# Performance work log

Measured on AMD Instinct MI355X. Metric: run time of the kernel, lower is better.

## Reference

```python
import jax, jax.numpy as jnp
import numpy as np

D_MODEL = 1024
NUM_SLOTS = 4096
MIN_K = 8
MAX_K = 32


def setup_inputs() -> dict:
    key = jax.random.key(0)
    k1, k2, k3 = jax.random.split(key, 3)
    x = jax.random.normal(k1, (4, 1024, D_MODEL), dtype=jnp.float32)
    param_pool = 0.02 * jax.random.normal(k2, (NUM_SLOTS, D_MODEL), dtype=jnp.float32)
    w_router = 0.02 * jax.random.normal(k3, (D_MODEL, NUM_SLOTS), dtype=jnp.float32)
    return {"x": x, "param_pool": param_pool, "w_router": w_router}


def _route(x, w_router):
    # Router: linear projection to slot logits, softmax, dynamic top-k in [MIN_K, MAX_K].
    logits = jnp.einsum('bsd,dn->bsn', x, w_router)           # [B,S,N]
    probs = jax.nn.softmax(logits, axis=-1)
    top_probs, indices = jax.lax.top_k(probs, MAX_K)          # [B,S,K]
    # dynamic k: always keep first MIN_K slots; keep up to MAX_K while prob > uniform
    pos = jnp.arange(MAX_K)
    keep = (pos < MIN_K) | (top_probs > (1.0 / NUM_SLOTS))    # [B,S,K] bool
    keep_f = keep.astype(top_probs.dtype)
    masked = top_probs * keep_f
    weights = masked / (jnp.sum(masked, axis=-1, keepdims=True) + 1e-9)
    # load-balancing aux loss: N * sum(mean_prob_per_slot * frac_tokens_routed_per_slot)
    mean_probs = jnp.mean(probs, axis=(0, 1))                 # [N]
    counts = jnp.zeros((NUM_SLOTS,), dtype=jnp.float32).at[indices.reshape(-1)].add(keep_f.reshape(-1))
    frac = counts / (jnp.sum(keep_f) + 1e-9)
    aux_loss = NUM_SLOTS * jnp.sum(mean_probs * frac)
    return indices, weights, keep, aux_loss


def reference(x, param_pool, w_router):
    indices, weights, keep, aux_loss = _route(x, w_router)
    selected_params = param_pool[indices]                      # [B,S,K,D] gather
    proj = jnp.einsum('bsd,bskd->bsk', x, selected_params)     # per-token dot scores
    weighted_proj = proj * weights
    output = jnp.einsum('bsk,bskd->bsd', weighted_proj, selected_params)
    flat_indices = indices.reshape(-1)
    flat_keep = keep.reshape(-1)
    touched = jnp.zeros((NUM_SLOTS,), dtype=jnp.bool_).at[flat_indices].max(flat_keep)
    active_count = jnp.sum(touched)
    return (output, aux_loss, active_count)
```

## Files before the change

### kernel.cpp

```cpp
#include <hip/hip_runtime.h>
#include <math.h>
#include <stdint.h>

#define D_MODEL   1024
#define NUM_SLOTS 4096
#define N_TOKENS  4096
#define MIN_K     8
#define MAX_K     32
#define KP        1024
#define NSTEP     32

typedef _Float16 f16x8 __attribute__((ext_vector_type(8)));
typedef _Float16 f16x4 __attribute__((ext_vector_type(4)));
typedef float    f32x4 __attribute__((ext_vector_type(4)));

__device__ __forceinline__ void gload16(const void* g, void* l) {
    __builtin_amdgcn_global_load_lds((const __attribute__((address_space(1))) void*)g,
                                     (__attribute__((address_space(3))) void*)l,
                                     16, 0, 0);
}

__device__ __forceinline__ uint32_t bf16rn(float f) {
    uint32_t u = __float_as_uint(f);
    return (u + 0x7FFFu + ((u >> 16) & 1u)) >> 16;
}

__device__ __forceinline__ uint32_t ford(float f) {
    uint32_t b = __float_as_uint(f);
    return b ^ (uint32_t)(((int32_t)b >> 31) | 0x80000000);
}

__global__ __launch_bounds__(256) void pack_all(const float* __restrict__ x,
                                                const float* __restrict__ w,
                                                const float* __restrict__ pool,
                                                _Float16* __restrict__ A,
                                                _Float16* __restrict__ BT,
                                                uint32_t* __restrict__ poolbf,
                                                float* __restrict__ clr,
                                                int* __restrict__ failcnt) {
    __shared__ float tile[64][65];
    const int bid = blockIdx.x;
    const int tid = threadIdx.x;

    if (bid < 4096) {
        if (bid < 32) clr[bid * 256 + tid] = 0.f;
        if (bid == 32 && tid == 0) *failcnt = 0;
        const int i = bid * 256 + tid;
        const float4 v = reinterpret_cast<const float4*>(x)[i];
        const int t = i >> 8;
        const int d = (i & 255) << 2;
        f16x4 hi;
        hi[0] = (_Float16)v.x; hi[1] = (_Float16)v.y;
        hi[2] = (_Float16)v.z; hi[3] = (_Float16)v.w;
        *(f16x4*)(A + (size_t)t * KP + d) = hi;
    } else if (bid < 5120) {
        const int b2 = bid - 4096;
        const int n0 = (b2 & 63) * 64;
        const int k0 = (b2 >> 6) * 64;
        {
            const int c  = tid & 63;
            const int r0 = tid >> 6;
#pragma unroll
            for (int i = 0; i < 16; ++i) {
                const int r = r0 * 16 + i;
                tile[r][c] = w[(size_t)(k0 + r) * NUM_SLOTS + n0 + c];
            }
        }
        __syncthreads();
        const int nl  = tid >> 2;
        const int kl0 = (tid & 3) * 16;
        _Float16* rowp = BT + (size_t)(n0 + nl) * KP + k0;
#pragma unroll
        for (int j4 = 0; j4 < 16; j4 += 4) {
            f16x4 hi;
#pragma unroll
            for (int u = 0; u < 4; ++u)
                hi[u] = (_Float16)tile[kl0 + j4 + u][nl];
            *(f16x4*)(rowp + kl0 + j4) = hi;
        }
    } else {
        const size_t i = (size_t)(bid - 5120) * 256 + tid;
        const float4* s4 = reinterpret_cast<const float4*>(pool);
        const float4 a = s4[2 * i];
        const float4 b = s4[2 * i + 1];
        uint4 u;
        u.x = bf16rn(a.x) | (bf16rn(a.y) << 16);
        u.y = bf16rn(a.z) | (bf16rn(a.w) << 16);
        u.z = bf16rn(b.x) | (bf16rn(b.y) << 16);
        u.w = bf16rn(b.z) | (bf16rn(b.w) << 16);
        reinterpret_cast<uint4*>(poolbf)[i] = u;
    }
}

#define STAGE_A(NXT, S2) \
    gload16(gA0 + (size_t)(S2) * 32, (void*)(AsF + (NXT) * 8192 + tid * 8)); \
    gload16(gA1 + (size_t)(S2) * 32, (void*)(AsF + (NXT) * 8192 + 4096 + tid * 8));
#define STAGE_B(NXT, S2) \
    gload16(gB0 + (size_t)(S2) * 32, (void*)(BsF + (NXT) * 8192 + tid * 8)); \
    gload16(gB1 + (size_t)(S2) * 32, (void*)(BsF + (NXT) * 8192 + 4096 + tid * 8));

#define MM(AF, M) \
    acc[M][0] = __builtin_amdgcn_mfma_f32_16x16x32_f16(AF, bf0, acc[M][0], 0, 0, 0); \
    acc[M][1] = __builtin_amdgcn_mfma_f32_16x16x32_f16(AF, bf1, acc[M][1], 0, 0, 0); \
    acc[M][2] = __builtin_amdgcn_mfma_f32_16x16x32_f16(AF, bf2, acc[M][2], 0, 0, 0); \
    acc[M][3] = __builtin_amdgcn_mfma_f32_16x16x32_f16(AF, bf3, acc[M][3], 0, 0, 0);

#define GSTEP(S, CUR, NXT) do { \
    const _Float16* a_ = AsF + (CUR) * 8192; \
    const _Float16* b_ = BsF + (CUR) * 8192; \
    f16x8 bf0 = *(const f16x8*)(b_ + offB0); \
    f16x8 bf1 = *(const f16x8*)(b_ + offB1); \
    f16x8 bf2 = *(const f16x8*)(b_ + offB2); \
    f16x8 bf3 = *(const f16x8*)(b_ + offB3); \
    f16x8 a0 = *(const f16x8*)(a_ + offA0); \
    f16x8 a1 = *(const f16x8*)(a_ + offA1); \
    f16x8 a2 = *(const f16x8*)(a_ + offA2); \
    f16x8 a3 = *(const f16x8*)(a_ + offA3); \
    if ((S) + 2 < NSTEP) { STAGE_A(NXT, (S) + 2) } \
    asm volatile("" ::: "memory"); \
    __builtin_amdgcn_s_barrier(); \
    __builtin_amdgcn_s_setprio(1); \
    MM(a0, 0) MM(a1, 1) MM(a2, 2) MM(a3, 3) \
    __builtin_amdgcn_s_setprio(0); \
    asm volatile("" ::: "memory"); \
    __builtin_amdgcn_s_barrier(); \
    a0 = *(const f16x8*)(a_ + offA4); \
    a1 = *(const f16x8*)(a_ + offA5); \
    a2 = *(const f16x8*)(a_ + offA6); \
    a3 = *(const f16x8*)(a_ + offA7); \
    if ((S) + 2 < NSTEP) { STAGE_B(NXT, (S) + 2) } \
    asm volatile("" ::: "memory"); \
    __builtin_amdgcn_s_barrier(); \
    __builtin_amdgcn_s_setprio(1); \
    MM(a0, 4) MM(a1, 5) MM(a2, 6) MM(a3, 7) \
    __builtin_amdgcn_s_setprio(0); \
    if ((S) < NSTEP - 2) { asm volatile("s_waitcnt vmcnt(4)" ::: "memory"); } \
    else                 { asm volatile("s_waitcnt vmcnt(0)" ::: "memory"); } \
    __builtin_amdgcn_s_barrier(); \
} while (0)

__global__ __launch_bounds__(512, 2) void gemm256(const _Float16* __restrict__ A,
                                                  const _Float16* __restrict__ BT,
                                                  float* __restrict__ C,
                                                  int nbm) {
    __shared__ _Float16 AsF[4 * 8192];
    __shared__ _Float16 BsF[4 * 8192];
    const int tid  = threadIdx.x;
    const int lane = tid & 63;
    const int wv   = tid >> 6;
    const int wm   = wv >> 2;
    const int wn   = wv & 3;

    int brow, bcol;
    {
        const int bid = blockIdx.x;
        if (nbm == 16) {
            const int xcd = bid & 7;
            const int l   = bid >> 3;
            brow = (xcd & 3) * 4 + (l & 3);
            bcol = (xcd >> 2) * 8 + (l >> 2);
        } else {
            brow = bid >> 4;
            bcol = bid & 15;
        }
    }
    const size_t bm = (size_t)brow * 256;
    const size_t bn = (size_t)bcol * 256;

    const int rowA = tid >> 2;
    const int slot = tid & 3;
    const int sswz = slot ^ ((rowA >> 1) & 3);
    const _Float16* gA0 = A  + (bm + rowA) * (size_t)KP + sswz * 8;
    const _Float16* gA1 = A  + (bm + rowA + 128) * (size_t)KP + sswz * 8;
    const _Float16* gB0 = BT + (bn + rowA) * (size_t)KP + sswz * 8;
    const _Float16* gB1 = BT + (bn + rowA + 128) * (size_t)KP + sswz * 8;

    int offA0, offA1, offA2, offA3, offA4, offA5, offA6, offA7;
    int offB0, offB1, offB2, offB3;
    {
        const int r15 = lane & 15, ls = lane >> 4;
#define AOFF(M) (((wm) * 128 + (M) * 16 + r15) * 32 + \
                 ((ls ^ ((((wm) * 128 + (M) * 16 + r15) >> 1) & 3)) * 8))
#define BOFF(N) (((wn) * 64 + (N) * 16 + r15) * 32 + \
                 ((ls ^ ((((wn) * 64 + (N) * 16 + r15) >> 1) & 3)) * 8))
        offA0 = AOFF(0); offA1 = AOFF(1); offA2 = AOFF(2); offA3 = AOFF(3);
        offA4 = AOFF(4); offA5 = AOFF(5); offA6 = AOFF(6); offA7 = AOFF(7);
        offB0 = BOFF(0); offB1 = BOFF(1); offB2 = BOFF(2); offB3 = BOFF(3);
#undef AOFF
#undef BOFF
    }

    f32x4 acc[8][4] = {};

    STAGE_A(0, 0) STAGE_B(0, 0)
    STAGE_A(1, 1) STAGE_B(1, 1)
    asm volatile("s_waitcnt vmcnt(4)" ::: "memory");
    __builtin_amdgcn_s_barrier();

    for (int s4 = 0; s4 < NSTEP; s4 += 4) {
        GSTEP(s4 + 0, 0, 2);
        GSTEP(s4 + 1, 1, 3);
        GSTEP(s4 + 2, 2, 0);
        GSTEP(s4 + 3, 3, 1);
    }

    const size_t crow = bm + wm * 128 + ((lane >> 4) << 2);
    const size_t ccol = bn + wn * 64 + (lane & 15);
#pragma unroll
    for (int m = 0; m < 8; ++m)
#pragma unroll
        for (int r = 0; r < 4; ++r) {
            float* cp = C + (crow + m * 16 + r) * (size_t)NUM_SLOTS + ccol;
#pragma unroll
            for (int n = 0; n < 4; ++n) cp[n * 16] = acc[m][n][r];
        }
}

#define RECOMP(G, A, B, Cc, D) do { \
    uint32_t t0 = (msk & (1u << (A)))  ? k##A  : 0u; \
    uint32_t t1 = (msk & (1u << (B)))  ? k##B  : 0u; \
    uint32_t t2 = (msk & (1u << (Cc))) ? k##Cc : 0u; \
    uint32_t t3 = (msk & (1u << (D)))  ? k##D  : 0u; \
    t0 = t0 > t1 ? t0 : t1; t2 = t2 > t3 ? t2 : t3; \
    gm##G = t0 > t2 ? t0 : t2; } while (0)

#define XROUND(IT) do { \
    uint32_t best = gm0; \
    if (gm1 > best) best = gm1; \
    if (gm2 > best) best = gm2; \
    if (gm3 > best) best = gm3; \
    uint32_t wb = best; \
    _Pragma("unroll") \
    for (int o = 32; o; o >>= 1) { \
        const uint32_t p = __shfl_xor(wb, o); \
        if (p > wb) wb = p; \
    } \
    if (lane == (IT)) kept = wb; \
    if (best == wb) { \
        const int idx = 4095 - (int)(wb & 0xFFFu); \
        const int rem = idx - kb; \
        const int jj = rem >> 8; \
        msk &= ~(1u << (4 * jj + (rem & 3))); \
        switch (jj) { \
            case 0:  RECOMP(0, 0, 1, 2, 3); break; \
            case 1:  RECOMP(1, 4, 5, 6, 7); break; \
            case 2:  RECOMP(2, 8, 9, 10, 11); break; \
            default: RECOMP(3, 12, 13, 14, 15); break; \
        } \
    } \
} while (0)

#define MAKEKEYS(E0, E1, E2, E3) \
    k0  = (ford((E0).x) & 0xFFFFF000u) | (uint32_t)(4095 - (kb + 0)); \
    k1  = (ford((E0).y) & 0xFFFFF000u) | (uint32_t)(4095 - (kb + 1)); \
    k2  = (ford((E0).z) & 0xFFFFF000u) | (uint32_t)(4095 - (kb + 2)); \
    k3  = (ford((E0).w) & 0xFFFFF000u) | (uint32_t)(4095 - (kb + 3)); \
    k4  = (ford((E1).x) & 0xFFFFF000u) | (uint32_t)(4095 - (kb + 256)); \
    k5  = (ford((E1).y) & 0xFFFFF000u) | (uint32_t)(4095 - (kb + 257)); \
    k6  = (ford((E1).z) & 0xFFFFF000u) | (uint32_t)(4095 - (kb + 258)); \
    k7  = (ford((E1).w) & 0xFFFFF000u) | (uint32_t)(4095 - (kb + 259)); \
    k8  = (ford((E2).x) & 0xFFFFF000u) | (uint32_t)(4095 - (kb + 512)); \
    k9  = (ford((E2).y) & 0xFFFFF000u) | (uint32_t)(4095 - (kb + 513)); \
    k10 = (ford((E2).z) & 0xFFFFF000u) | (uint32_t)(4095 - (kb + 514)); \
    k11 = (ford((E2).w) & 0xFFFFF000u) | (uint32_t)(4095 - (kb + 515)); \
    k12 = (ford((E3).x) & 0xFFFFF000u) | (uint32_t)(4095 - (kb + 768)); \
    k13 = (ford((E3).y) & 0xFFFFF000u) | (uint32_t)(4095 - (kb + 769)); \
    k14 = (ford((E3).z) & 0xFFFFF000u) | (uint32_t)(4095 - (kb + 770)); \
    k15 = (ford((E3).w) & 0xFFFFF000u) | (uint32_t)(4095 - (kb + 771));

#define UNPK8(q, a0,a1,a2,a3,a4,a5,a6,a7) \
    a0 = __uint_as_float((q).x << 16); a1 = __uint_as_float((q).x & 0xFFFF0000u); \
    a2 = __uint_as_float((q).y << 16); a3 = __uint_as_float((q).y & 0xFFFF0000u); \
    a4 = __uint_as_float((q).z << 16); a5 = __uint_as_float((q).z & 0xFFFF0000u); \
    a6 = __uint_as_float((q).w << 16); a7 = __uint_as_float((q).w & 0xFFFF0000u);

#define PROJ_AND_OUT(TOK) do { \
    const float4* x4 = reinterpret_cast<const float4*>(x + (size_t)(TOK) * D_MODEL); \
    const float4 xa0 = x4[2 * lane]; \
    const float4 xb0 = x4[2 * lane + 1]; \
    const float4 xa1 = x4[2 * lane + 128]; \
    const float4 xb1 = x4[2 * lane + 129]; \
    float4 oa0 = {0,0,0,0}, ob0 = {0,0,0,0}, oa1 = {0,0,0,0}, ob1 = {0,0,0,0}; \
    _Pragma("unroll") \
    for (int ii = 0; ii < 8; ++ii) { \
        const int   i     = w * 8 + ii; \
        const int   slotg = __shfl(slotv, i); \
        const float wgt   = __shfl(wgtl, i); \
        if (wgt != 0.f) { \
            const uint4* pr = reinterpret_cast<const uint4*>(poolbf + (size_t)slotg * (D_MODEL / 2)); \
            const uint4 q0 = pr[lane]; \
            const uint4 q1 = pr[lane + 64]; \
            float pA0,pA1,pA2,pA3,pA4,pA5,pA6,pA7; \
            float pB0,pB1,pB2,pB3,pB4,pB5,pB6,pB7; \
            UNPK8(q0, pA0,pA1,pA2,pA3,pA4,pA5,pA6,pA7) \
            UNPK8(q1, pB0,pB1,pB2,pB3,pB4,pB5,pB6,pB7) \
            float d; \
            d = xa0.x * pA0; \
            d = fmaf(xa0.y, pA1, d); d = fmaf(xa0.z, pA2, d); d = fmaf(xa0.w, pA3, d); \
            d = fmaf(xb0.x, pA4, d); d = fmaf(xb0.y, pA5, d); d = fmaf(xb0.z, pA6, d); d = fmaf(xb0.w, pA7, d); \
            d = fmaf(xa1.x, pB0, d); d = fmaf(xa1.y, pB1, d); d = fmaf(xa1.z, pB2, d); d = fmaf(xa1.w, pB3, d); \
            d = fmaf(xb1.x, pB4, d); d = fmaf(xb1.y, pB5, d); d = fmaf(xb1.z, pB6, d); d = fmaf(xb1.w, pB7, d); \
            _Pragma("unroll") \
            for (int o = 32; o; o >>= 1) d += __shfl_xor(d, o); \
            const float wp = d * wgt; \
            oa0.x = fmaf(wp, pA0, oa0.x); oa0.y = fmaf(wp, pA1, oa0.y); \
            oa0.z = fmaf(wp, pA2, oa0.z); oa0.w = fmaf(wp, pA3, oa0.w); \
            ob0.x = fmaf(wp, pA4, ob0.x); ob0.y = fmaf(wp, pA5, ob0.y); \
            ob0.z = fmaf(wp, pA6, ob0.z); ob0.w = fmaf(wp, pA7, ob0.w); \
            oa1.x = fmaf(wp, pB0, oa1.x); oa1.y = fmaf(wp, pB1, oa1.y); \
            oa1.z = fmaf(wp, pB2, oa1.z); oa1.w = fmaf(wp, pB3, oa1.w); \
            ob1.x = fmaf(wp, pB4, ob1.x); ob1.y = fmaf(wp, pB5, ob1.y); \
            ob1.z = fmaf(wp, pB6, ob1.z); ob1.w = fmaf(wp, pB7, ob1.w); \
        } \
    } \
    { \
        float4* op = reinterpret_cast<float4*>(s_union + w * 1024); \
        op[2 * lane]       = oa0; \
        op[2 * lane + 1]   = ob0; \
        op[2 * lane + 128] = oa1; \
        op[2 * lane + 129] = ob1; \
    } \
    __syncthreads(); \
    float4 r = {0, 0, 0, 0}; \
    _Pragma("unroll") \
    for (int ww = 0; ww < 4; ++ww) { \
        const float4 vv = reinterpret_cast<const float4*>(s_union + ww * 1024)[tid]; \
        r.x += vv.x; r.y += vv.y; r.z += vv.z; r.w += vv.w; \
    } \
    reinterpret_cast<float4*>(out + (size_t)(TOK) * D_MODEL)[tid] = r; \
} while (0)

__global__ __launch_bounds__(256) void router_kernel(
    const float* __restrict__ logits,
    const float* __restrict__ x,
    const uint32_t* __restrict__ poolbf,
    float* __restrict__ out,
    float2* __restrict__ minv,
    float* __restrict__ counts,
    int* __restrict__ failcnt,
    int* __restrict__ faillist) {
    __shared__ float    s_union[NUM_SLOTS];
    __shared__ uint32_t s_cand[68];
    __shared__ float    s_redv[4];

    const int tid  = threadIdx.x;
    const int w    = tid >> 6;
    const int lane = tid & 63;
    const int wseg = w << 10;
    const int t    = blockIdx.x;

    const float4* lrow4 =
        reinterpret_cast<const float4*>(logits + (size_t)t * NUM_SLOTS + wseg);

    float4 lv0, lv1, lv2, lv3;
    lv0 = lrow4[lane];
    lv1 = lrow4[lane + 64];
    lv2 = lrow4[lane + 128];
    lv3 = lrow4[lane + 192];
    reinterpret_cast<float4*>(s_union + wseg)[lane]       = lv0;
    reinterpret_cast<float4*>(s_union + wseg)[lane + 64]  = lv1;
    reinterpret_cast<float4*>(s_union + wseg)[lane + 128] = lv2;
    reinterpret_cast<float4*>(s_union + wseg)[lane + 192] = lv3;
    float lmax = fmaxf(fmaxf(fmaxf(lv0.x, lv0.y), fmaxf(lv0.z, lv0.w)),
                       fmaxf(fmaxf(lv1.x, lv1.y), fmaxf(lv1.z, lv1.w)));
    lmax = fmaxf(lmax, fmaxf(fmaxf(lv2.x, lv2.y), fmaxf(lv2.z, lv2.w)));
    lmax = fmaxf(lmax, fmaxf(fmaxf(lv3.x, lv3.y), fmaxf(lv3.z, lv3.w)));
#pragma unroll
    for (int o = 32; o; o >>= 1) lmax = fmaxf(lmax, __shfl_xor(lmax, o));
    if (lane == 0) s_redv[w] = lmax;
    __syncthreads();
    const float m = fmaxf(fmaxf(s_redv[0], s_redv[1]), fmaxf(s_redv[2], s_redv[3]));
    __syncthreads();

    float lsum;
    {
        float4 ev0, ev1, ev2, ev3;
        ev0.x = __expf(lv0.x - m); ev0.y = __expf(lv0.y - m);
        ev0.z = __expf(lv0.z - m); ev0.w = __expf(lv0.w - m);
        ev1.x = __expf(lv1.x - m); ev1.y = __expf(lv1.y - m);
        ev1.z = __expf(lv1.z - m); ev1.w = __expf(lv1.w - m);
        ev2.x = __expf(lv2.x - m); ev2.y = __expf(lv2.y - m);
        ev2.z = __expf(lv2.z - m); ev2.w = __expf(lv2.w - m);
        ev3.x = __expf(lv3.x - m); ev3.y = __expf(lv3.y - m);
        ev3.z = __expf(lv3.z - m); ev3.w = __expf(lv3.w - m);
        lsum = (ev0.x + ev0.y + ev0.z + ev0.w) + (ev1.x + ev1.y + ev1.z + ev1.w) +
               (ev2.x + ev2.y + ev2.z + ev2.w) + (ev3.x + ev3.y + ev3.z + ev3.w);
    }
#pragma unroll
    for (int o = 32; o; o >>= 1) lsum += __shfl_xor(lsum, o);
    if (lane == 0) s_redv[w] = lsum;
    __syncthreads();
    const float inv = 1.0f / (s_redv[0] + s_redv[1] + s_redv[2] + s_redv[3]);
    if (tid == 0) minv[t] = make_float2(m, inv);

    const int kb = wseg + 4 * lane;
    uint32_t k0, k1, k2, k3, k4, k5, k6, k7;
    uint32_t k8, k9, k10, k11, k12, k13, k14, k15;
    MAKEKEYS(lv0, lv1, lv2, lv3)

    uint32_t msk = 0xFFFFu;
    uint32_t gm0, gm1, gm2, gm3;
    RECOMP(0, 0, 1, 2, 3); RECOMP(1, 4, 5, 6, 7);
    RECOMP(2, 8, 9, 10, 11); RECOMP(3, 12, 13, 14, 15);

    uint32_t kept = 0;
    for (int it = 0; it < 16; ++it) { XROUND(it); }

    {
        uint32_t best = gm0;
        if (gm1 > best) best = gm1;
        if (gm2 > best) best = gm2;
        if (gm3 > best) best = gm3;
#pragma unroll
        for (int o = 32; o; o >>= 1) {
            const uint32_t p = __shfl_xor(best, o);
            if (p > best) best = p;
        }
        if (lane == 0) s_cand[64 + w] = best;
    }
    if (lane < 16) s_cand[w * 16 + lane] = kept;
    __syncthreads();

    uint32_t v0 = s_cand[lane];
#pragma unroll
    for (int k = 2; k <= 64; k <<= 1) {
#pragma unroll
        for (int j = k >> 1; j > 0; j >>= 1) {
            const bool jl = (lane & j) == 0;
            const uint32_t p = __shfl_xor(v0, j);
            const bool km = ((lane & k) == 0) == jl;
            v0 = ((p > v0) == km) ? p : v0;
        }
    }

    const uint32_t th = __shfl(v0, 31);
    uint32_t mw = s_cand[64];
    {
        const uint32_t m1 = s_cand[65], m2 = s_cand[66], m3 = s_cand[67];
        if (m1 > mw) mw = m1;
        if (m2 > mw) mw = m2;
        if (m3 > mw) mw = m3;
    }
    if (th < mw) {
        if (tid == 0) {
            const int fi = atomicAdd(failcnt, 1);
            faillist[fi] = t;
        }
        return;
    }

    const int slotv = 4095 - (int)(v0 & 0xFFFu);
    float pv = 0.f;
    if (lane < 32) pv = __expf(s_union[slotv] - m) * inv;
    const bool kp = (lane < MIN_K) || (pv > (1.0f / 4096.0f));
    float wsum = kp ? pv : 0.f;
#pragma unroll
    for (int o = 32; o; o >>= 1) wsum += __shfl_xor(wsum, o);
    const float wgtl = kp ? pv / (wsum + 1e-9f) : 0.f;
    if (w == 0 && lane < 32 && kp) atomicAdd(&counts[slotv], 1.0f);
    __syncthreads();

    PROJ_AND_OUT(t);
}

__global__ __launch_bounds__(256) void router_fixup(
    const float* __restrict__ logits,
    const float* __restrict__ x,
    const uint32_t* __restrict__ poolbf,
    float* __restrict__ out,
    const float2* __restrict__ minv,
    float* __restrict__ counts,
    const int* __restrict__ failcnt,
    const int* __restrict__ faillist) {
    __shared__ float    s_union[NUM_SLOTS];
    __shared__ uint32_t s_cand[128];

    const int tid  = threadIdx.x;
    const int w    = tid >> 6;
    const int lane = tid & 63;
    const int wseg = w << 10;
    const int n    = failcnt[0];

    for (int fi = blockIdx.x; fi < n; fi += gridDim.x) {
        const int t = faillist[fi];
        const float4* lrow4 =
            reinterpret_cast<const float4*>(logits + (size_t)t * NUM_SLOTS + wseg);
        const float4 lv0 = lrow4[lane];
        const float4 lv1 = lrow4[lane + 64];
        const float4 lv2 = lrow4[lane + 128];
        const float4 lv3 = lrow4[lane + 192];
        reinterpret_cast<float4*>(s_union + wseg)[lane]       = lv0;
        reinterpret_cast<float4*>(s_union + wseg)[lane + 64]  = lv1;
        reinterpret_cast<float4*>(s_union + wseg)[lane + 128] = lv2;
        reinterpret_cast<float4*>(s_union + wseg)[lane + 192] = lv3;
        const float2 mv = minv[t];
        const float m = mv.x, inv = mv.y;

        const int kb = wseg + 4 * lane;
        uint32_t k0, k1, k2, k3, k4, k5, k6, k7;
        uint32_t k8, k9, k10, k11, k12, k13, k14, k15;
        MAKEKEYS(lv0, lv1, lv2, lv3)

        uint32_t msk = 0xFFFFu;
        uint32_t gm0, gm1, gm2, gm3;
        RECOMP(0, 0, 1, 2, 3); RECOMP(1, 4, 5, 6, 7);
        RECOMP(2, 8, 9, 10, 11); RECOMP(3, 12, 13, 14, 15);

        uint32_t kept = 0;
        for (int it = 0; it < 32; ++it) { XROUND(it); }
        if (lane < 32) s_cand[w * 32 + lane] = kept;
        __syncthreads();

        uint32_t v0 = s_cand[lane];
        uint32_t v1 = s_cand[64 + lane];
#pragma unroll
        for (int k = 2; k <= 128; k <<= 1) {
#pragma unroll
            for (int j = k >> 1; j > 0; j >>= 1) {
                if (j == 64) {
                    const uint32_t a = v0 > v1 ? v0 : v1;
                    const uint32_t b = v0 > v1 ? v1 : v0;
                    v0 = a; v1 = b;
                } else {
                    const bool jl = (lane & j) == 0;
                    {
                        const uint32_t p = __shfl_xor(v0, j);
                        const bool km = ((lane & k) == 0) == jl;
                        v0 = ((p > v0) == km) ? p : v0;
                    }
                    {
                        const uint32_t p = __shfl_xor(v1, j);
                        const bool km = (((lane + 64) & k) == 0) == jl;
                        v1 = ((p > v1) == km) ? p : v1;
                    }
                }
            }
        }

        const int slotv = 4095 - (int)(v0 & 0xFFFu);
        float pv = 0.f;
        if (lane < 32) pv = __expf(s_union[slotv] - m) * inv;
        const bool kp = (lane < MIN_K) || (pv > (1.0f / 4096.0f));
        float wsum = kp ? pv : 0.f;
#pragma unroll
        for (int o = 32; o; o >>= 1) wsum += __shfl_xor(wsum, o);
        const float wgtl = kp ? pv / (wsum + 1e-9f) : 0.f;
        if (w == 0 && lane < 32 && kp) atomicAdd(&counts[slotv], 1.0f);
        __syncthreads();

        PROJ_AND_OUT(t);
        __syncthreads();
    }
}

__global__ __launch_bounds__(256) void colsum_lg(const float* __restrict__ logits,
                                                 const float2* __restrict__ minv,
                                                 float* __restrict__ colsum) {
    const int tid = threadIdx.x;
    const int s0  = blockIdx.x * 1024;
    const int t0  = blockIdx.y * 64;
    float a0 = 0.f, a1 = 0.f, a2 = 0.f, a3 = 0.f;
    for (int t = 0; t < 64; ++t) {
        const float2 mv = minv[t0 + t];
        const float4 v = reinterpret_cast<const float4*>(
            logits + (size_t)(t0 + t) * NUM_SLOTS + s0)[tid];
        a0 = fmaf(__expf(v.x - mv.x), mv.y, a0);
        a1 = fmaf(__expf(v.y - mv.x), mv.y, a1);
        a2 = fmaf(__expf(v.z - mv.x), mv.y, a2);
        a3 = fmaf(__expf(v.w - mv.x), mv.y, a3);
    }
    const int c = s0 + 4 * tid;
    atomicAdd(&colsum[c + 0], a0);
    atomicAdd(&colsum[c + 1], a1);
    atomicAdd(&colsum[c + 2], a2);
    atomicAdd(&colsum[c + 3], a3);
}

__global__ __launch_bounds__(256) void finalize_kernel(
    const float* __restrict__ counts,
    const float* __restrict__ colsum,
    float* __restrict__ out2) {
    __shared__ float s_tot[4], s_act[4], s_dot[4];
    const int tid = threadIdx.x;
    float tot = 0.f, act = 0.f, dot = 0.f;
#pragma unroll
    for (int j = 0; j < 16; ++j) {
        const int i = j * 256 + tid;
        const float c = counts[i];
        tot += c;
        act += (c > 0.f) ? 1.f : 0.f;
        dot += colsum[i] * c;
    }
#pragma unroll
    for (int o = 32; o; o >>= 1) {
        tot += __shfl_xor(tot, o);
        act += __shfl_xor(act, o);
        dot += __shfl_xor(dot, o);
    }
    if ((tid & 63) == 0) {
        s_tot[tid >> 6] = tot; s_act[tid >> 6] = act; s_dot[tid >> 6] = dot;
    }
    __syncthreads();
    if (tid == 0) {
        const float T  = s_tot[0] + s_tot[1] + s_tot[2] + s_tot[3];
        const float A  = s_act[0] + s_act[1] + s_act[2] + s_act[3];
        const float Dt = s_dot[0] + s_dot[1] + s_dot[2] + s_dot[3];
        out2[0] = Dt / (T + 1e-9f);
        out2[1] = A;
    }
}

extern "C" void kernel_launch(void* const* d_in, const int* in_sizes, int n_in,
                              void* d_out, int out_size, void* d_ws, size_t ws_size,
                              hipStream_t stream) {
    const float* x    = (const float*)d_in[0];
    const float* pool = (const float*)d_in[1];
    const float* w    = (const float*)d_in[2];
    float* out = (float*)d_out;

    const size_t MB = 1024 * 1024;
    char* ws = (char*)d_ws;
    float*     colsum   = (float*)ws;
    float*     counts   = (float*)(ws + 16 * 1024);
    float2*    minv     = (float2*)(ws + 32 * 1024);
    int*       failcnt  = (int*)(ws + 64 * 1024);
    int*       faillist = (int*)(ws + 68 * 1024);
    uint32_t*  poolbf   = (uint32_t*)(ws + 128 * 1024);
    _Float16*  Apack    = (_Float16*)(ws + 128 * 1024 + 8 * MB);
    _Float16*  Bpack    = (_Float16*)(ws + 128 * 1024 + 16 * MB);
    float*     logits   = (float*)(ws + 128 * 1024 + 24 * MB);

    pack_all<<<7168, 256, 0, stream>>>(x, w, pool, Apack, Bpack, poolbf,
                                       colsum, failcnt);

    gemm256<<<16 * 16, 512, 0, stream>>>(Apack, Bpack, logits, 16);

    router_kernel<<<N_TOKENS, 256, 0, stream>>>(logits, x, poolbf, out,
                                                minv, counts, failcnt, faillist);

    router_fixup<<<64, 256, 0, stream>>>(logits, x, poolbf, out,
                                         minv, counts, failcnt, faillist);

    colsum_lg<<<dim3(NUM_SLOTS / 1024, N_TOKENS / 64), 256, 0, stream>>>(
        logits, minv, colsum);

    finalize_kernel<<<1, 256, 0, stream>>>(counts, colsum, out + (out_size - 2));
}
```

Before: 149.4 us.

## Merge fixup, column-sum and finalize kernels into one launch with last-block reduction

Combines router_fixup, colsum_lg and finalize_kernel into a single kernel. The first 256 blocks compute softmax column sums and the remaining 64 handle fallback tokens. The last block to finish, detected with an atomic counter, performs the aux-loss and active-count reduction. This removes two kernel launches and their serialization gaps, and lets colsum work overlap with fixup work. In exchange it adds a threadfence/atomic completion pattern and a larger shared-memory footprint for the colsum blocks.

```diff
diff --git a/kernel.cpp b/kernel.cpp
--- a/kernel.cpp
+++ b/kernel.cpp
@@ -44,7 +44,7 @@
 
     if (bid < 4096) {
         if (bid < 32) clr[bid * 256 + tid] = 0.f;
-        if (bid == 32 && tid == 0) *failcnt = 0;
+        if (bid == 32 && tid == 0) { failcnt[0] = 0; failcnt[1] = 0; }
         const int i = bid * 256 + tid;
         const float4 v = reinterpret_cast<const float4*>(x)[i];
         const int t = i >> 8;
@@ -463,150 +463,155 @@
     PROJ_AND_OUT(t);
 }
 
-__global__ __launch_bounds__(256) void router_fixup(
+#define CSFX_BLOCKS 320
+
+__global__ __launch_bounds__(256) void colsum_fx(
     const float* __restrict__ logits,
     const float* __restrict__ x,
     const uint32_t* __restrict__ poolbf,
     float* __restrict__ out,
     const float2* __restrict__ minv,
     float* __restrict__ counts,
-    const int* __restrict__ failcnt,
-    const int* __restrict__ faillist) {
+    float* __restrict__ colsum,
+    int* __restrict__ failcnt,
+    const int* __restrict__ faillist,
+    float* __restrict__ out2) {
     __shared__ float    s_union[NUM_SLOTS];
     __shared__ uint32_t s_cand[128];
-
+    __shared__ float    s_tot[4], s_act[4], s_dot[4];
+    __shared__ int      s_last;
+
+    const int bid  = blockIdx.x;
     const int tid  = threadIdx.x;
     const int w    = tid >> 6;
     const int lane = tid & 63;
-    const int wseg = w << 10;
-    const int n    = failcnt[0];
-
-    for (int fi = blockIdx.x; fi < n; fi += gridDim.x) {
-        const int t = faillist[fi];
-        const float4* lrow4 =
-            reinterpret_cast<const float4*>(logits + (size_t)t * NUM_SLOTS + wseg);
-        const float4 lv0 = lrow4[lane];
-        const float4 lv1 = lrow4[lane + 64];
-        const float4 lv2 = lrow4[lane + 128];
-        const float4 lv3 = lrow4[lane + 192];
-        reinterpret_cast<float4*>(s_union + wseg)[lane]       = lv0;
-        reinterpret_cast<float4*>(s_union + wseg)[lane + 64]  = lv1;
-        reinterpret_cast<float4*>(s_union + wseg)[lane + 128] = lv2;
-        reinterpret_cast<float4*>(s_union + wseg)[lane + 192] = lv3;
-        const float2 mv = minv[t];
-        const float m = mv.x, inv = mv.y;
-
-        const int kb = wseg + 4 * lane;
-        uint32_t k0, k1, k2, k3, k4, k5, k6, k7;
-        uint32_t k8, k9, k10, k11, k12, k13, k14, k15;
-        MAKEKEYS(lv0, lv1, lv2, lv3)
-
-        uint32_t msk = 0xFFFFu;
-        uint32_t gm0, gm1, gm2, gm3;
-        RECOMP(0, 0, 1, 2, 3); RECOMP(1, 4, 5, 6, 7);
-        RECOMP(2, 8, 9, 10, 11); RECOMP(3, 12, 13, 14, 15);
-
-        uint32_t kept = 0;
-        for (int it = 0; it < 32; ++it) { XROUND(it); }
-        if (lane < 32) s_cand[w * 32 + lane] = kept;
-        __syncthreads();
-
-        uint32_t v0 = s_cand[lane];
-        uint32_t v1 = s_cand[64 + lane];
-#pragma unroll
-        for (int k = 2; k <= 128; k <<= 1) {
-#pragma unroll
-            for (int j = k >> 1; j > 0; j >>= 1) {
-                if (j == 64) {
-                    const uint32_t a = v0 > v1 ? v0 : v1;
-                    const uint32_t b = v0 > v1 ? v1 : v0;
-                    v0 = a; v1 = b;
-                } else {
-                    const bool jl = (lane & j) == 0;
-                    {
-                        const uint32_t p = __shfl_xor(v0, j);
-                        const bool km = ((lane & k) == 0) == jl;
-                        v0 = ((p > v0) == km) ? p : v0;
-                    }
-                    {
-                        const uint32_t p = __shfl_xor(v1, j);
-                        const bool km = (((lane + 64) & k) == 0) == jl;
-                        v1 = ((p > v1) == km) ? p : v1;
+
+    if (bid < 256) {
+        const int s0 = (bid & 3) * 1024;
+        const int t0 = (bid >> 2) * 64;
+        float a0 = 0.f, a1 = 0.f, a2 = 0.f, a3 = 0.f;
+        for (int t = 0; t < 64; ++t) {
+            const float2 mv = minv[t0 + t];
+            const float4 v = reinterpret_cast<const float4*>(
+                logits + (size_t)(t0 + t) * NUM_SLOTS + s0)[tid];
+            a0 = fmaf(__expf(v.x - mv.x), mv.y, a0);
+            a1 = fmaf(__expf(v.y - mv.x), mv.y, a1);
+            a2 = fmaf(__expf(v.z - mv.x), mv.y, a2);
+            a3 = fmaf(__expf(v.w - mv.x), mv.y, a3);
+        }
+        const int c = s0 + 4 * tid;
+        atomicAdd(&colsum[c + 0], a0);
+        atomicAdd(&colsum[c + 1], a1);
+        atomicAdd(&colsum[c + 2], a2);
+        atomicAdd(&colsum[c + 3], a3);
+    } else {
+        const int wseg = w << 10;
+        const int n = failcnt[0];
+        for (int fi = bid - 256; fi < n; fi += 64) {
+            const int t = faillist[fi];
+            const float4* lrow4 =
+                reinterpret_cast<const float4*>(logits + (size_t)t * NUM_SLOTS + wseg);
+            const float4 lv0 = lrow4[lane];
+            const float4 lv1 = lrow4[lane + 64];
+            const float4 lv2 = lrow4[lane + 128];
+            const float4 lv3 = lrow4[lane + 192];
+            reinterpret_cast<float4*>(s_union + wseg)[lane]       = lv0;
+            reinterpret_cast<float4*>(s_union + wseg)[lane + 64]  = lv1;
+            reinterpret_cast<float4*>(s_union + wseg)[lane + 128] = lv2;
+            reinterpret_cast<float4*>(s_union + wseg)[lane + 192] = lv3;
+            const float2 mv = minv[t];
+            const float m = mv.x, inv = mv.y;
+
+            const int kb = wseg + 4 * lane;
+            uint32_t k0, k1, k2, k3, k4, k5, k6, k7;
+            uint32_t k8, k9, k10, k11, k12, k13, k14, k15;
+            MAKEKEYS(lv0, lv1, lv2, lv3)
+
+            uint32_t msk = 0xFFFFu;
+            uint32_t gm0, gm1, gm2, gm3;
+            RECOMP(0, 0, 1, 2, 3); RECOMP(1, 4, 5, 6, 7);
+            RECOMP(2, 8, 9, 10, 11); RECOMP(3, 12, 13, 14, 15);
+
+            uint32_t kept = 0;
+            for (int it = 0; it < 32; ++it) { XROUND(it); }
+            if (lane < 32) s_cand[w * 32 + lane] = kept;
+            __syncthreads();
+
+            uint32_t v0 = s_cand[lane];
+            uint32_t v1 = s_cand[64 + lane];
+#pragma unroll
+            for (int k = 2; k <= 128; k <<= 1) {
+#pragma unroll
+                for (int j = k >> 1; j > 0; j >>= 1) {
+                    if (j == 64) {
+                        const uint32_t a = v0 > v1 ? v0 : v1;
+                        const uint32_t b = v0 > v1 ? v1 : v0;
+                        v0 = a; v1 = b;
+                    } else {
+                        const bool jl = (lane & j) == 0;
+                        {
+                            const uint32_t p = __shfl_xor(v0, j);
+                            const bool km = ((lane & k) == 0) == jl;
+                            v0 = ((p > v0) == km) ? p : v0;
+                        }
+                        {
+                            const uint32_t p = __shfl_xor(v1, j);
+                            const bool km = (((lane + 64) & k) == 0) == jl;
+                            v1 = ((p > v1) == km) ? p : v1;
+                        }
                     }
                 }
             }
-        }
-
-        const int slotv = 4095 - (int)(v0 & 0xFFFu);
-        float pv = 0.f;
-        if (lane < 32) pv = __expf(s_union[slotv] - m) * inv;
-        const bool kp = (lane < MIN_K) || (pv > (1.0f / 4096.0f));
-        float wsum = kp ? pv : 0.f;
-#pragma unroll
-        for (int o = 32; o; o >>= 1) wsum += __shfl_xor(wsum, o);
-        const float wgtl = kp ? pv / (wsum + 1e-9f) : 0.f;
-        if (w == 0 && lane < 32 && kp) atomicAdd(&counts[slotv], 1.0f);
+
+            const int slotv = 4095 - (int)(v0 & 0xFFFu);
+            float pv = 0.f;
+            if (lane < 32) pv = __expf(s_union[slotv] - m) * inv;
+            const bool kp = (lane < MIN_K) || (pv > (1.0f / 4096.0f));
+            float wsum = kp ? pv : 0.f;
+#pragma unroll
+            for (int o = 32; o; o >>= 1) wsum += __shfl_xor(wsum, o);
+            const float wgtl = kp ? pv / (wsum + 1e-9f) : 0.f;
+            if (w == 0 && lane < 32 && kp) atomicAdd(&counts[slotv], 1.0f);
+            __syncthreads();
+
+            PROJ_AND_OUT(t);
+            __syncthreads();
+        }
+    }
+
+    __threadfence();
+    __syncthreads();
+    if (tid == 0) s_last = (atomicAdd(&failcnt[1], 1) == CSFX_BLOCKS - 1) ? 1 : 0;
+    __syncthreads();
+    if (s_last) {
+        __threadfence();
+        float tot = 0.f, act = 0.f, dot = 0.f;
+#pragma unroll
+        for (int j = 0; j < 16; ++j) {
+            const int i = j * 256 + tid;
+            const float c  = atomicAdd(&counts[i], 0.f);
+            const float cs = atomicAdd(&colsum[i], 0.f);
+            tot += c;
+            act += (c > 0.f) ? 1.f : 0.f;
+            dot += cs * c;
+        }
+#pragma unroll
+        for (int o = 32; o; o >>= 1) {
+            tot += __shfl_xor(tot, o);
+            act += __shfl_xor(act, o);
+            dot += __shfl_xor(dot, o);
+        }
+        if ((tid & 63) == 0) {
+            s_tot[tid >> 6] = tot; s_act[tid >> 6] = act; s_dot[tid >> 6] = dot;
+        }
         __syncthreads();
-
-        PROJ_AND_OUT(t);
-        __syncthreads();
-    }
-}
-
-__global__ __launch_bounds__(256) void colsum_lg(const float* __restrict__ logits,
-                                                 const float2* __restrict__ minv,
-                                                 float* __restrict__ colsum) {
-    const int tid = threadIdx.x;
-    const int s0  = blockIdx.x * 1024;
-    const int t0  = blockIdx.y * 64;
-    float a0 = 0.f, a1 = 0.f, a2 = 0.f, a3 = 0.f;
-    for (int t = 0; t < 64; ++t) {
-        const float2 mv = minv[t0 + t];
-        const float4 v = reinterpret_cast<const float4*>(
-            logits + (size_t)(t0 + t) * NUM_SLOTS + s0)[tid];
-        a0 = fmaf(__expf(v.x - mv.x), mv.y, a0);
-        a1 = fmaf(__expf(v.y - mv.x), mv.y, a1);
-        a2 = fmaf(__expf(v.z - mv.x), mv.y, a2);
-        a3 = fmaf(__expf(v.w - mv.x), mv.y, a3);
-    }
-    const int c = s0 + 4 * tid;
-    atomicAdd(&colsum[c + 0], a0);
-    atomicAdd(&colsum[c + 1], a1);
-    atomicAdd(&colsum[c + 2], a2);
-    atomicAdd(&colsum[c + 3], a3);
-}
-
-__global__ __launch_bounds__(256) void finalize_kernel(
-    const float* __restrict__ counts,
-    const float* __restrict__ colsum,
-    float* __restrict__ out2) {
-    __shared__ float s_tot[4], s_act[4], s_dot[4];
-    const int tid = threadIdx.x;
-    float tot = 0.f, act = 0.f, dot = 0.f;
-#pragma unroll
-    for (int j = 0; j < 16; ++j) {
-        const int i = j * 256 + tid;
-        const float c = counts[i];
-        tot += c;
-        act += (c > 0.f) ? 1.f : 0.f;
-        dot += colsum[i] * c;
-    }
-#pragma unroll
-    for (int o = 32; o; o >>= 1) {
-        tot += __shfl_xor(tot, o);
-        act += __shfl_xor(act, o);
-        dot += __shfl_xor(dot, o);
-    }
-    if ((tid & 63) == 0) {
-        s_tot[tid >> 6] = tot; s_act[tid >> 6] = act; s_dot[tid >> 6] = dot;
-    }
-    __syncthreads();
-    if (tid == 0) {
-        const float T  = s_tot[0] + s_tot[1] + s_tot[2] + s_tot[3];
-        const float A  = s_act[0] + s_act[1] + s_act[2] + s_act[3];
-        const float Dt = s_dot[0] + s_dot[1] + s_dot[2] + s_dot[3];
-        out2[0] = Dt / (T + 1e-9f);
-        out2[1] = A;
+        if (tid == 0) {
+            const float T  = s_tot[0] + s_tot[1] + s_tot[2] + s_tot[3];
+            const float A  = s_act[0] + s_act[1] + s_act[2] + s_act[3];
+            const float Dt = s_dot[0] + s_dot[1] + s_dot[2] + s_dot[3];
+            out2[0] = Dt / (T + 1e-9f);
+            out2[1] = A;
+        }
     }
 }
 
@@ -638,11 +643,7 @@
     router_kernel<<<N_TOKENS, 256, 0, stream>>>(logits, x, poolbf, out,
                                                 minv, counts, failcnt, faillist);
 
-    router_fixup<<<64, 256, 0, stream>>>(logits, x, poolbf, out,
-                                         minv, counts, failcnt, faillist);
-
-    colsum_lg<<<dim3(NUM_SLOTS / 1024, N_TOKENS / 64), 256, 0, stream>>>(
-        logits, minv, colsum);
-
-    finalize_kernel<<<1, 256, 0, stream>>>(counts, colsum, out + (out_size - 2));
-}
+    colsum_fx<<<CSFX_BLOCKS, 256, 0, stream>>>(logits, x, poolbf, out, minv,
+                                               counts, colsum, failcnt,
+                                               faillist, out + (out_size - 2));
+}
```

After: 160.8 us. +7.6%, slower.
